# Kernel optimization log

Measured on AMD Instinct MI355X. Metric: run time of the kernel, lower is better.

The kernel has to match this reference:

```python
import jax, jax.numpy as jnp
import numpy as np

EPS = 1e-12  # matches torch F.normalize eps


def _l2n(x, axis):
    return x / jnp.maximum(jnp.linalg.norm(x, axis=axis, keepdims=True), EPS)


def setup_inputs() -> dict:
    key = jax.random.key(0)
    k1, k2, k3 = jax.random.split(key, 3)
    x = jax.random.normal(k1, (4, 128, 30, 40), dtype=jnp.float32)
    conv_w = jax.random.normal(k2, (64, 128), dtype=jnp.float32) * 0.02  # 1x1 conv, no bias (vladv2=False)
    centroids = jax.random.uniform(k3, (64, 128), dtype=jnp.float32)
    return {"x": x, "conv_w": conv_w, "centroids": centroids}


def reference(x, conv_w, centroids):
    N, C, H, W = x.shape
    K = centroids.shape[0]
    ps, stride = 4, 1  # patch_sizes='4', strides='1'

    # descriptor-wise L2 normalization of input
    x = _l2n(x, 1)

    # 1x1 conv + softmax over clusters -> soft assignment [N,K,H,W]
    soft_assign = jax.nn.softmax(jnp.einsum('kc,nchw->nkhw', conv_w, x), axis=1)

    # weighted residuals [N,K,C,H,W] (vectorized form of the per-cluster loop)
    res = (x[:, None] - centroids[None, :, :, None, None]) * soft_assign[:, :, None]

    # global VLAD: sum over spatial, intra-norm, flatten, L2-norm
    vlad_global = res.sum(axis=(-1, -2))            # [N,K,C]
    vlad_global = _l2n(vlad_global, 2).reshape(N, K * C)
    vlad_global = _l2n(vlad_global, 1)

    # integral image over spatial dims with zero pad on top/left
    r = res.reshape(N, K * C, H, W)
    integ = jnp.cumsum(jnp.cumsum(r, axis=-1), axis=-2)
    integ = jnp.pad(integ, ((0, 0), (0, 0), (1, 0), (1, 0)))  # [N,KC,H+1,W+1]

    # dilated 2x2 box-filter conv == 4-corner integral-image lookup
    TL = integ[:, :, :H + 1 - ps:stride, :W + 1 - ps:stride]
    TR = integ[:, :, :H + 1 - ps:stride, ps::stride]
    BL = integ[:, :, ps::stride, :W + 1 - ps:stride]
    BR = integ[:, :, ps::stride, ps::stride]
    vl = (TL - TR - BL + BR) / (ps * ps)            # [N,KC,Hp,Wp]
    Hp, Wp = vl.shape[-2], vl.shape[-1]

    # local VLAD: intra-norm over descriptor dim, then global L2 per patch
    vl = vl.reshape(N, K, C, Hp * Wp)
    vl = _l2n(vl, 2).reshape(N, K * C, Hp * Wp)
    vlad_local = _l2n(vl, 1)

    return vlad_global, vlad_local
```

## Files before the change

### kernel.cpp

```cpp
#include <hip/hip_runtime.h>
#include <math.h>

#define EPSV 1e-12f

namespace {
constexpr int N_  = 4;
constexpr int C_  = 128;
constexpr int H_  = 30;
constexpr int W_  = 40;
constexpr int K_  = 64;
constexpr int HW_ = H_ * W_;
constexpr int HP_ = 27;
constexpr int WP_ = 37;
constexpr int P_  = HP_ * WP_;
constexpr int KC_ = K_ * C_;
constexpr int CP_ = C_ * P_;
constexpr int CS_ = HP_ * W_;
constexpr int SL_ = CS_ / 4;
}

static __device__ __forceinline__ float4 ld4(const float* p) {
    return *reinterpret_cast<const float4*>(p);
}

__global__ __launch_bounds__(256) void k1_norm_softmax(
    const float* __restrict__ x, const float* __restrict__ conv_w,
    float* __restrict__ xnT, float* __restrict__ xnP, float* __restrict__ sa)
{
    __shared__ float xrow[C_ * W_];
    __shared__ float conv_s[K_ * C_];
    __shared__ float invn[W_];
    __shared__ float s_s[K_ * W_];

    const int b = blockIdx.x;
    const int n = b / H_, h = b - n * H_;
    const int t = threadIdx.x;

    for (int i = t; i < C_ * W_; i += 256) {
        const int c = i / W_, w = i - c * W_;
        xrow[i] = x[(size_t)(n * C_ + c) * HW_ + h * W_ + w];
    }
    for (int i = t; i < K_ * C_; i += 256) conv_s[i] = conv_w[i];
    __syncthreads();

    if (t < W_) {
        float s = 0.f;
        for (int c = 0; c < C_; ++c) { const float v = xrow[c * W_ + t]; s += v * v; }
        invn[t] = 1.f / fmaxf(sqrtf(s), EPSV);
    }
    __syncthreads();

    for (int i = t; i < C_ * W_; i += 256) {
        const int c = i / W_, w = i - c * W_;
        const float v = xrow[i] * invn[w];
        xrow[i] = v;
        xnT[(size_t)(n * C_ + c) * HW_ + h * W_ + w] = v;
    }
    __syncthreads();

    for (int i = t; i < W_ * C_; i += 256) {
        const int w = i / C_, c = i - w * C_;
        xnP[((size_t)n * HW_ + h * W_ + w) * C_ + c] = xrow[c * W_ + w];
    }

    for (int d = t; d < K_ * W_; d += 256) {
        const int k = d / W_, w = d - k * W_;
        const float* cw = &conv_s[k * C_];
        float s = 0.f;
        for (int c = 0; c < C_; ++c) s += cw[c] * xrow[c * W_ + w];
        s_s[d] = s;
    }
    __syncthreads();

    if (t < W_) {
        const int w = t;
        float m = -1e30f;
        for (int k = 0; k < K_; ++k) m = fmaxf(m, s_s[k * W_ + w]);
        float sum = 0.f;
        for (int k = 0; k < K_; ++k) sum += expf(s_s[k * W_ + w] - m);
        const float inv = 1.f / sum;
        for (int k = 0; k < K_; ++k)
            sa[(size_t)(n * K_ + k) * HW_ + h * W_ + w] = expf(s_s[k * W_ + w] - m) * inv;
    }
}

__global__ __launch_bounds__(1024) void k2_vg(
    const float* __restrict__ sa, const float* __restrict__ xnP,
    const float* __restrict__ cent, float* __restrict__ vg_u,
    float* __restrict__ vg_r)
{
    const int b = blockIdx.x;
    const int n = b >> 6, k = b & 63;
    const int t = threadIdx.x;
    const int c = t & 127, eighth = t >> 7;
    constexpr int CHW = HW_ / 8;

    const float* sarow = &sa[(size_t)b * HW_ + eighth * CHW];
    const float* xp = &xnP[((size_t)n * HW_ + eighth * CHW) * C_ + c];
    float g0 = 0.f, g1 = 0.f, b0 = 0.f, b1 = 0.f;
    for (int pix = 0; pix < CHW; pix += 2) {
        const float s0 = sarow[pix + 0], s1 = sarow[pix + 1];
        g0 += s0 * xp[(size_t)(pix + 0) * C_];
        g1 += s1 * xp[(size_t)(pix + 1) * C_];
        b0 += s0; b1 += s1;
    }
    const float g  = g0 + g1;
    const float bs = b0 + b1;

    __shared__ float gs[1024], bss[1024];
    __shared__ float red[2];
    gs[t] = g; bss[t] = bs;
    __syncthreads();

    float vg = 0.f;
    if (t < 128) {
        float gt = 0.f, bt = 0.f;
#pragma unroll
        for (int e = 0; e < 8; ++e) { gt += gs[t + 128 * e]; bt += bss[t + 128 * e]; }
        vg = gt - cent[k * C_ + t] * bt;
        float nsq = vg * vg;
        for (int off = 32; off >= 1; off >>= 1) nsq += __shfl_down(nsq, off);
        if ((t & 63) == 0) red[t >> 6] = nsq;
    }
    __syncthreads();
    const float tot  = red[0] + red[1];
    const float norm = sqrtf(tot);
    const float iv   = 1.f / fmaxf(norm, EPSV);
    if (t < 128) vg_u[(size_t)b * C_ + t] = vg * iv;
    if (t == 0) { const float rr = norm * iv; vg_r[b] = rr * rr; }
}

__global__ __launch_bounds__(256) void k3_vg_fin(
    const float* __restrict__ vg_u, const float* __restrict__ vg_r,
    float* __restrict__ out)
{
    const int n = blockIdx.x;
    const int t = threadIdx.x;
    __shared__ float inv2s;
    if (t == 0) {
        float s = 0.f;
        for (int k = 0; k < K_; ++k) s += vg_r[n * K_ + k];
        inv2s = 1.f / fmaxf(sqrtf(s), EPSV);
    }
    __syncthreads();
    const float inv2 = inv2s;
    for (int i = t; i < KC_; i += 256)
        out[(size_t)n * KC_ + i] = vg_u[(size_t)n * KC_ + i] * inv2;
}

#define COLSUM_VEC_T(cs_q, sa_s, x0, x1, x2, x3)                                \
    for (int s = t; s < SL_; s += 256) {                                        \
        const int i = s * 4;                                                    \
        const float4 sa0 = ld4(&sa_s[i]);                                       \
        const float4 sa1 = ld4(&sa_s[i + W_]);                                  \
        const float4 sa2 = ld4(&sa_s[i + 2 * W_]);                              \
        const float4 sa3 = ld4(&sa_s[i + 3 * W_]);                              \
        float acc[4][4];                                                        \
        const float* xc[4] = {x0, x1, x2, x3};                                  \
        _Pragma("unroll")                                                       \
        for (int ch = 0; ch < 4; ++ch) {                                        \
            const float4 a0 = ld4(xc[ch] + i);                                  \
            const float4 a1 = ld4(xc[ch] + i + W_);                             \
            const float4 a2 = ld4(xc[ch] + i + 2 * W_);                         \
            const float4 a3 = ld4(xc[ch] + i + 3 * W_);                         \
            acc[0][ch] = sa0.x * a0.x + sa1.x * a1.x + sa2.x * a2.x + sa3.x * a3.x; \
            acc[1][ch] = sa0.y * a0.y + sa1.y * a1.y + sa2.y * a2.y + sa3.y * a3.y; \
            acc[2][ch] = sa0.z * a0.z + sa1.z * a1.z + sa2.z * a2.z + sa3.z * a3.z; \
            acc[3][ch] = sa0.w * a0.w + sa1.w * a1.w + sa2.w * a2.w + sa3.w * a3.w; \
        }                                                                       \
        _Pragma("unroll")                                                       \
        for (int q = 0; q < 4; ++q)                                             \
            cs_q[q][s] = make_float4(acc[q][0], acc[q][1], acc[q][2], acc[q][3]); \
    }

static __device__ __forceinline__ float4 csget(const float4 cs_q[4][SL_], int e) {
    return cs_q[e & 3][e >> 2];
}

__global__ __launch_bounds__(256) void k4_norm(
    const float* __restrict__ sa, const float* __restrict__ xnT,
    const float* __restrict__ cent, float* __restrict__ nsqp)
{
    __shared__ float  sa_s[HW_];
    __shared__ float  B_s[P_];
    __shared__ float4 cs_q[4][SL_];

    const int b  = blockIdx.x;
    const int cq = b & 3;
    const int nk = b >> 2;
    const int n  = nk >> 6, k = nk & 63;
    const int t  = threadIdx.x;

    for (int i = t; i < HW_; i += 256) sa_s[i] = sa[(size_t)nk * HW_ + i];
    __syncthreads();
    for (int p = t; p < P_; p += 256) {
        const int hp = p / WP_, wp = p - hp * WP_;
        float bs = 0.f;
#pragma unroll
        for (int dh = 0; dh < 4; ++dh) {
            const float* r = &sa_s[(hp + dh) * W_ + wp];
            bs += r[0] + r[1] + r[2] + r[3];
        }
        B_s[p] = bs;
    }

    float nsq0 = 0.f, nsq1 = 0.f, nsq2 = 0.f, nsq3 = 0.f;
    const float* xb = xnT + (size_t)n * C_ * HW_;

    for (int g = 0; g < 8; ++g) {
        const int c0 = cq * 32 + g * 4;
        const float* x0 = xb + (size_t)(c0 + 0) * HW_;
        const float* x1 = xb + (size_t)(c0 + 1) * HW_;
        const float* x2 = xb + (size_t)(c0 + 2) * HW_;
        const float* x3 = xb + (size_t)(c0 + 3) * HW_;
        __syncthreads();
        COLSUM_VEC_T(cs_q, sa_s, x0, x1, x2, x3)
        __syncthreads();
        const float4 ce = ld4(&cent[k * C_ + c0]);
#pragma unroll
        for (int pi = 0; pi < 4; ++pi) {
            const int p = t + pi * 256;
            if (p < P_) {
                const int hp = p / WP_, wp = p - hp * WP_;
                const int base = hp * W_ + wp;
                const float4 s0 = csget(cs_q, base);
                const float4 s1 = csget(cs_q, base + 1);
                const float4 s2 = csget(cs_q, base + 2);
                const float4 s3 = csget(cs_q, base + 3);
                const float Bv = B_s[p];
                const float ux = (s0.x + s1.x + s2.x + s3.x) - ce.x * Bv;
                const float uy = (s0.y + s1.y + s2.y + s3.y) - ce.y * Bv;
                const float uz = (s0.z + s1.z + s2.z + s3.z) - ce.z * Bv;
                const float uw = (s0.w + s1.w + s2.w + s3.w) - ce.w * Bv;
                const float add = ux * ux + uy * uy + uz * uz + uw * uw;
                if      (pi == 0) nsq0 += add;
                else if (pi == 1) nsq1 += add;
                else if (pi == 2) nsq2 += add;
                else              nsq3 += add;
            }
        }
    }
#pragma unroll
    for (int pi = 0; pi < 4; ++pi) {
        const int p = t + pi * 256;
        if (p < P_) {
            const float v = (pi == 0 ? nsq0 : pi == 1 ? nsq1 : pi == 2 ? nsq2 : nsq3);
            nsqp[(size_t)b * P_ + p] = v * 0.00390625f;
        }
    }
}

__global__ __launch_bounds__(256) void k5_combine(
    const float* __restrict__ nsqp, float* __restrict__ inv1,
    float* __restrict__ rloc)
{
    const int nk = blockIdx.x;
    const int t  = threadIdx.x;
    for (int p = t; p < P_; p += 256) {
        const float s = nsqp[(size_t)(nk * 4 + 0) * P_ + p]
                      + nsqp[(size_t)(nk * 4 + 1) * P_ + p]
                      + nsqp[(size_t)(nk * 4 + 2) * P_ + p]
                      + nsqp[(size_t)(nk * 4 + 3) * P_ + p];
        const float norm = sqrtf(s);
        const float iv = 1.f / fmaxf(norm, EPSV);
        inv1[(size_t)nk * P_ + p] = iv * 0.0625f;
        const float rr = norm * iv;
        rloc[(size_t)nk * P_ + p] = rr * rr;
    }
}

__global__ __launch_bounds__(256) void k6_inv2(
    const float* __restrict__ rloc, float* __restrict__ inv2)
{
    const int n = blockIdx.x >> 2;
    const int p = (blockIdx.x & 3) * 256 + threadIdx.x;
    if (p < P_) {
        float s = 0.f;
        for (int k = 0; k < K_; ++k) s += rloc[(size_t)(n * K_ + k) * P_ + p];
        inv2[n * P_ + p] = 1.f / fmaxf(sqrtf(s), EPSV);
    }
}

__global__ __launch_bounds__(256) void k7_write(
    const float* __restrict__ sa, const float* __restrict__ xnT,
    const float* __restrict__ cent, const float* __restrict__ inv1,
    const float* __restrict__ inv2, float* __restrict__ outl)
{
    __shared__ float  sa_s[HW_];
    __shared__ float  scl_s[P_];
    __shared__ float  t2_s[P_];
    __shared__ float4 cs_q[4][SL_];

    const int b  = blockIdx.x;
    const int cq = b & 3;
    const int nk = b >> 2;
    const int n  = nk >> 6, k = nk & 63;
    const int t  = threadIdx.x;

    for (int i = t; i < HW_; i += 256) sa_s[i] = sa[(size_t)nk * HW_ + i];
    __syncthreads();
    for (int p = t; p < P_; p += 256) {
        const int hp = p / WP_, wp = p - hp * WP_;
        float bs = 0.f;
#pragma unroll
        for (int dh = 0; dh < 4; ++dh) {
            const float* r = &sa_s[(hp + dh) * W_ + wp];
            bs += r[0] + r[1] + r[2] + r[3];
        }
        const float sc = inv1[(size_t)nk * P_ + p] * inv2[n * P_ + p];
        scl_s[p] = sc;
        t2_s[p]  = bs * sc;
    }

    const float* xb = xnT + (size_t)n * C_ * HW_;
    float* ob = outl + (size_t)nk * CP_;

    for (int g = 0; g < 8; ++g) {
        const int c0 = cq * 32 + g * 4;
        const float* x0 = xb + (size_t)(c0 + 0) * HW_;
        const float* x1 = xb + (size_t)(c0 + 1) * HW_;
        const float* x2 = xb + (size_t)(c0 + 2) * HW_;
        const float* x3 = xb + (size_t)(c0 + 3) * HW_;
        __syncthreads();
        COLSUM_VEC_T(cs_q, sa_s, x0, x1, x2, x3)
        __syncthreads();
        const float4 ce = ld4(&cent[k * C_ + c0]);
#pragma unroll
        for (int pi = 0; pi < 4; ++pi) {
            const int p = t + pi * 256;
            if (p < P_) {
                const int hp = p / WP_, wp = p - hp * WP_;
                const int base = hp * W_ + wp;
                const float4 s0 = csget(cs_q, base);
                const float4 s1 = csget(cs_q, base + 1);
                const float4 s2 = csget(cs_q, base + 2);
                const float4 s3 = csget(cs_q, base + 3);
                const float sc = scl_s[p];
                const float tt = t2_s[p];
                ob[(size_t)(c0 + 0) * P_ + p] = (s0.x + s1.x + s2.x + s3.x) * sc - ce.x * tt;
                ob[(size_t)(c0 + 1) * P_ + p] = (s0.y + s1.y + s2.y + s3.y) * sc - ce.y * tt;
                ob[(size_t)(c0 + 2) * P_ + p] = (s0.z + s1.z + s2.z + s3.z) * sc - ce.z * tt;
                ob[(size_t)(c0 + 3) * P_ + p] = (s0.w + s1.w + s2.w + s3.w) * sc - ce.w * tt;
            }
        }
    }
}

extern "C" void kernel_launch(void* const* d_in, const int* in_sizes, int n_in,
                              void* d_out, int out_size, void* d_ws, size_t ws_size,
                              hipStream_t stream)
{
    const float* x      = (const float*)d_in[0];
    const float* conv_w = (const float*)d_in[1];
    const float* cent   = (const float*)d_in[2];
    float* out = (float*)d_out;
    float* ws  = (float*)d_ws;

    float* xnT  = ws;
    float* xnP  = ws + 614400;
    float* sa   = ws + 1228800;
    float* vg_u = ws + 1536000;
    float* vg_r = ws + 1568768;
    float* nsqp = ws + 1569024;
    float* inv1 = ws + 2592000;
    float* rloc = ws + 2847744;
    float* inv2 = ws + 3103488;

    float* outl = out + (size_t)N_ * KC_;

    k1_norm_softmax<<<N_ * H_, 256, 0, stream>>>(x, conv_w, xnT, xnP, sa);
    k2_vg<<<N_ * K_, 1024, 0, stream>>>(sa, xnP, cent, vg_u, vg_r);
    k3_vg_fin<<<N_, 256, 0, stream>>>(vg_u, vg_r, out);
    k4_norm<<<N_ * K_ * 4, 256, 0, stream>>>(sa, xnT, cent, nsqp);
    k5_combine<<<N_ * K_, 256, 0, stream>>>(nsqp, inv1, rloc);
    k6_inv2<<<N_ * 4, 256, 0, stream>>>(rloc, inv2);
    k7_write<<<N_ * K_ * 4, 256, 0, stream>>>(sa, xnT, cent, inv1, inv2, outl);
}
```

Measured before the change: 126.1 us.

## Merge global VLAD kernels into norm kernels and vectorize local output stores

The global-VLAD reduction (formerly its own 1024-thread kernel) now runs as 256 extra blocks inside the local-norm kernel. The global finalization runs as 4 extra blocks inside the combine kernel, which removes two launches and lets independent work share the GPU. The write kernel regroups its channels as stride-4 interleaves so each thread computes four consecutive patches and writes them as float4 stores, with a scalar tail for the leftovers. This trades per-launch overhead and scalar stores for heavier register use and more complex indexing.

```diff
diff --git a/kernel.cpp b/kernel.cpp
--- a/kernel.cpp
+++ b/kernel.cpp
@@ -82,70 +82,6 @@
         for (int k = 0; k < K_; ++k)
             sa[(size_t)(n * K_ + k) * HW_ + h * W_ + w] = expf(s_s[k * W_ + w] - m) * inv;
     }
-}
-
-__global__ __launch_bounds__(1024) void k2_vg(
-    const float* __restrict__ sa, const float* __restrict__ xnP,
-    const float* __restrict__ cent, float* __restrict__ vg_u,
-    float* __restrict__ vg_r)
-{
-    const int b = blockIdx.x;
-    const int n = b >> 6, k = b & 63;
-    const int t = threadIdx.x;
-    const int c = t & 127, eighth = t >> 7;
-    constexpr int CHW = HW_ / 8;
-
-    const float* sarow = &sa[(size_t)b * HW_ + eighth * CHW];
-    const float* xp = &xnP[((size_t)n * HW_ + eighth * CHW) * C_ + c];
-    float g0 = 0.f, g1 = 0.f, b0 = 0.f, b1 = 0.f;
-    for (int pix = 0; pix < CHW; pix += 2) {
-        const float s0 = sarow[pix + 0], s1 = sarow[pix + 1];
-        g0 += s0 * xp[(size_t)(pix + 0) * C_];
-        g1 += s1 * xp[(size_t)(pix + 1) * C_];
-        b0 += s0; b1 += s1;
-    }
-    const float g  = g0 + g1;
-    const float bs = b0 + b1;
-
-    __shared__ float gs[1024], bss[1024];
-    __shared__ float red[2];
-    gs[t] = g; bss[t] = bs;
-    __syncthreads();
-
-    float vg = 0.f;
-    if (t < 128) {
-        float gt = 0.f, bt = 0.f;
-#pragma unroll
-        for (int e = 0; e < 8; ++e) { gt += gs[t + 128 * e]; bt += bss[t + 128 * e]; }
-        vg = gt - cent[k * C_ + t] * bt;
-        float nsq = vg * vg;
-        for (int off = 32; off >= 1; off >>= 1) nsq += __shfl_down(nsq, off);
-        if ((t & 63) == 0) red[t >> 6] = nsq;
-    }
-    __syncthreads();
-    const float tot  = red[0] + red[1];
-    const float norm = sqrtf(tot);
-    const float iv   = 1.f / fmaxf(norm, EPSV);
-    if (t < 128) vg_u[(size_t)b * C_ + t] = vg * iv;
-    if (t == 0) { const float rr = norm * iv; vg_r[b] = rr * rr; }
-}
-
-__global__ __launch_bounds__(256) void k3_vg_fin(
-    const float* __restrict__ vg_u, const float* __restrict__ vg_r,
-    float* __restrict__ out)
-{
-    const int n = blockIdx.x;
-    const int t = threadIdx.x;
-    __shared__ float inv2s;
-    if (t == 0) {
-        float s = 0.f;
-        for (int k = 0; k < K_; ++k) s += vg_r[n * K_ + k];
-        inv2s = 1.f / fmaxf(sqrtf(s), EPSV);
-    }
-    __syncthreads();
-    const float inv2 = inv2s;
-    for (int i = t; i < KC_; i += 256)
-        out[(size_t)n * KC_ + i] = vg_u[(size_t)n * KC_ + i] * inv2;
 }
 
 #define COLSUM_VEC_T(cs_q, sa_s, x0, x1, x2, x3)                                \
@@ -177,19 +113,63 @@
     return cs_q[e & 3][e >> 2];
 }
 
-__global__ __launch_bounds__(256) void k4_norm(
+__global__ __launch_bounds__(256) void k4_merged(
     const float* __restrict__ sa, const float* __restrict__ xnT,
-    const float* __restrict__ cent, float* __restrict__ nsqp)
+    const float* __restrict__ xnP, const float* __restrict__ cent,
+    float* __restrict__ nsqp, float* __restrict__ vg_u,
+    float* __restrict__ vg_r)
 {
     __shared__ float  sa_s[HW_];
     __shared__ float  B_s[P_];
     __shared__ float4 cs_q[4][SL_];
-
-    const int b  = blockIdx.x;
+    __shared__ float  gs[256], bss[256];
+    __shared__ float  red[2];
+
+    const int t = threadIdx.x;
+
+    if (blockIdx.x < 256) {
+        const int b = blockIdx.x;
+        const int n = b >> 6, k = b & 63;
+        const int c = t & 127, half = t >> 7;
+        constexpr int HHW = HW_ / 2;
+
+        const float* sarow = &sa[(size_t)b * HW_ + half * HHW];
+        const float* xp = &xnP[((size_t)n * HW_ + half * HHW) * C_ + c];
+        float g0 = 0.f, g1 = 0.f, g2 = 0.f, g3 = 0.f;
+        float b0 = 0.f, b1 = 0.f, b2 = 0.f, b3 = 0.f;
+        for (int pix = 0; pix < HHW; pix += 4) {
+            const float s0 = sarow[pix + 0], s1 = sarow[pix + 1];
+            const float s2 = sarow[pix + 2], s3 = sarow[pix + 3];
+            g0 += s0 * xp[(size_t)(pix + 0) * C_];
+            g1 += s1 * xp[(size_t)(pix + 1) * C_];
+            g2 += s2 * xp[(size_t)(pix + 2) * C_];
+            g3 += s3 * xp[(size_t)(pix + 3) * C_];
+            b0 += s0; b1 += s1; b2 += s2; b3 += s3;
+        }
+        gs[t]  = (g0 + g1) + (g2 + g3);
+        bss[t] = (b0 + b1) + (b2 + b3);
+        __syncthreads();
+
+        float vg = 0.f;
+        if (t < 128) {
+            vg = (gs[t] + gs[t + 128]) - cent[k * C_ + c] * (bss[t] + bss[t + 128]);
+            float nsq = vg * vg;
+            for (int off = 32; off >= 1; off >>= 1) nsq += __shfl_down(nsq, off);
+            if ((t & 63) == 0) red[t >> 6] = nsq;
+        }
+        __syncthreads();
+        const float tot  = red[0] + red[1];
+        const float norm = sqrtf(tot);
+        const float iv   = 1.f / fmaxf(norm, EPSV);
+        if (t < 128) vg_u[(size_t)b * C_ + t] = vg * iv;
+        if (t == 0) { const float rr = norm * iv; vg_r[b] = rr * rr; }
+        return;
+    }
+
+    const int b  = blockIdx.x - 256;
     const int cq = b & 3;
     const int nk = b >> 2;
     const int n  = nk >> 6, k = nk & 63;
-    const int t  = threadIdx.x;
 
     for (int i = t; i < HW_; i += 256) sa_s[i] = sa[(size_t)nk * HW_ + i];
     __syncthreads();
@@ -250,12 +230,27 @@
     }
 }
 
-__global__ __launch_bounds__(256) void k5_combine(
+__global__ __launch_bounds__(256) void k5_merged(
     const float* __restrict__ nsqp, float* __restrict__ inv1,
-    float* __restrict__ rloc)
-{
+    float* __restrict__ rloc, const float* __restrict__ vg_u,
+    const float* __restrict__ vg_r, float* __restrict__ out)
+{
+    const int t = threadIdx.x;
+    if (blockIdx.x >= 256) {
+        const int n = blockIdx.x - 256;
+        __shared__ float inv2s;
+        if (t == 0) {
+            float s = 0.f;
+            for (int k = 0; k < K_; ++k) s += vg_r[n * K_ + k];
+            inv2s = 1.f / fmaxf(sqrtf(s), EPSV);
+        }
+        __syncthreads();
+        const float inv2 = inv2s;
+        for (int i = t; i < KC_; i += 256)
+            out[(size_t)n * KC_ + i] = vg_u[(size_t)n * KC_ + i] * inv2;
+        return;
+    }
     const int nk = blockIdx.x;
-    const int t  = threadIdx.x;
     for (int p = t; p < P_; p += 256) {
         const float s = nsqp[(size_t)(nk * 4 + 0) * P_ + p]
                       + nsqp[(size_t)(nk * 4 + 1) * P_ + p]
@@ -316,32 +311,60 @@
     float* ob = outl + (size_t)nk * CP_;
 
     for (int g = 0; g < 8; ++g) {
-        const int c0 = cq * 32 + g * 4;
+        const int m = g & 3, h8 = g >> 2;
+        const int c0 = cq * 32 + h8 * 16 + m;
         const float* x0 = xb + (size_t)(c0 + 0) * HW_;
-        const float* x1 = xb + (size_t)(c0 + 1) * HW_;
-        const float* x2 = xb + (size_t)(c0 + 2) * HW_;
-        const float* x3 = xb + (size_t)(c0 + 3) * HW_;
+        const float* x1 = xb + (size_t)(c0 + 4) * HW_;
+        const float* x2 = xb + (size_t)(c0 + 8) * HW_;
+        const float* x3 = xb + (size_t)(c0 + 12) * HW_;
         __syncthreads();
         COLSUM_VEC_T(cs_q, sa_s, x0, x1, x2, x3)
         __syncthreads();
-        const float4 ce = ld4(&cent[k * C_ + c0]);
+        const float ce0 = cent[k * C_ + c0];
+        const float ce1 = cent[k * C_ + c0 + 4];
+        const float ce2 = cent[k * C_ + c0 + 8];
+        const float ce3 = cent[k * C_ + c0 + 12];
+        float* ob0 = ob + (size_t)(c0 + 0) * P_;
+        float* ob1 = ob + (size_t)(c0 + 4) * P_;
+        float* ob2 = ob + (size_t)(c0 + 8) * P_;
+        float* ob3 = ob + (size_t)(c0 + 12) * P_;
+
+        if (t < 249) {
+            const int p0 = m + t * 4;
+            float4 v0, v1, v2, v3;
 #pragma unroll
-        for (int pi = 0; pi < 4; ++pi) {
-            const int p = t + pi * 256;
-            if (p < P_) {
+            for (int pi = 0; pi < 4; ++pi) {
+                const int p = p0 + pi;
                 const int hp = p / WP_, wp = p - hp * WP_;
                 const int base = hp * W_ + wp;
                 const float4 s0 = csget(cs_q, base);
                 const float4 s1 = csget(cs_q, base + 1);
                 const float4 s2 = csget(cs_q, base + 2);
                 const float4 s3 = csget(cs_q, base + 3);
-                const float sc = scl_s[p];
-                const float tt = t2_s[p];
-                ob[(size_t)(c0 + 0) * P_ + p] = (s0.x + s1.x + s2.x + s3.x) * sc - ce.x * tt;
-                ob[(size_t)(c0 + 1) * P_ + p] = (s0.y + s1.y + s2.y + s3.y) * sc - ce.y * tt;
-                ob[(size_t)(c0 + 2) * P_ + p] = (s0.z + s1.z + s2.z + s3.z) * sc - ce.z * tt;
-                ob[(size_t)(c0 + 3) * P_ + p] = (s0.w + s1.w + s2.w + s3.w) * sc - ce.w * tt;
+                const float sc = scl_s[p], tt = t2_s[p];
+                reinterpret_cast<float*>(&v0)[pi] = (s0.x + s1.x + s2.x + s3.x) * sc - ce0 * tt;
+                reinterpret_cast<float*>(&v1)[pi] = (s0.y + s1.y + s2.y + s3.y) * sc - ce1 * tt;
+                reinterpret_cast<float*>(&v2)[pi] = (s0.z + s1.z + s2.z + s3.z) * sc - ce2 * tt;
+                reinterpret_cast<float*>(&v3)[pi] = (s0.w + s1.w + s2.w + s3.w) * sc - ce3 * tt;
             }
+            *reinterpret_cast<float4*>(ob0 + p0) = v0;
+            *reinterpret_cast<float4*>(ob1 + p0) = v1;
+            *reinterpret_cast<float4*>(ob2 + p0) = v2;
+            *reinterpret_cast<float4*>(ob3 + p0) = v3;
+        } else if (t < 252) {
+            const int u = t - 249;
+            const int p = (u < m) ? u : 996 + u;
+            const int hp = p / WP_, wp = p - hp * WP_;
+            const int base = hp * W_ + wp;
+            const float4 s0 = csget(cs_q, base);
+            const float4 s1 = csget(cs_q, base + 1);
+            const float4 s2 = csget(cs_q, base + 2);
+            const float4 s3 = csget(cs_q, base + 3);
+            const float sc = scl_s[p], tt = t2_s[p];
+            ob0[p] = (s0.x + s1.x + s2.x + s3.x) * sc - ce0 * tt;
+            ob1[p] = (s0.y + s1.y + s2.y + s3.y) * sc - ce1 * tt;
+            ob2[p] = (s0.z + s1.z + s2.z + s3.z) * sc - ce2 * tt;
+            ob3[p] = (s0.w + s1.w + s2.w + s3.w) * sc - ce3 * tt;
         }
     }
 }
@@ -369,10 +392,9 @@
     float* outl = out + (size_t)N_ * KC_;
 
     k1_norm_softmax<<<N_ * H_, 256, 0, stream>>>(x, conv_w, xnT, xnP, sa);
-    k2_vg<<<N_ * K_, 1024, 0, stream>>>(sa, xnP, cent, vg_u, vg_r);
-    k3_vg_fin<<<N_, 256, 0, stream>>>(vg_u, vg_r, out);
-    k4_norm<<<N_ * K_ * 4, 256, 0, stream>>>(sa, xnT, cent, nsqp);
-    k5_combine<<<N_ * K_, 256, 0, stream>>>(nsqp, inv1, rloc);
+    k4_merged<<<256 + N_ * K_ * 4, 256, 0, stream>>>(sa, xnT, xnP, cent,
+                                                     nsqp, vg_u, vg_r);
+    k5_merged<<<256 + N_, 256, 0, stream>>>(nsqp, inv1, rloc, vg_u, vg_r, out);
     k6_inv2<<<N_ * 4, 256, 0, stream>>>(rloc, inv2);
     k7_write<<<N_ * K_ * 4, 256, 0, stream>>>(sa, xnT, cent, inv1, inv2, outl);
 }
```

Result: faster. 123.1 us (-2.4%).
